# Kernel tuning notes

Measured on AMD Instinct MI355X. Metric: run time of the kernel, lower is better.

The kernel has to match this reference:

```python
import jax, jax.numpy as jnp
import numpy as np

BS, SEQ, ML, DEPTH = 32, 50, 16, 4
NN = 2 ** DEPTH - 1          # 15 nodes per complete binary tree (heap layout)
VOCAB, EMB, ENC = 50000, 128, 128
GH = 32                      # bigru hidden per direction
NC = 100                     # num_concepts
LH = 128                     # LSTM hidden
LIN = 2 + 2 * GH + NC + 1    # 167 LSTM feature dim


def _gru_dir(x, Wx, Wh, bx, bh, reverse):
    # x: [B, T, I]; torch GRU gate order r,z,n
    B, H = x.shape[0], Wh.shape[1]
    xe = jnp.einsum('bti,gi->btg', x, Wx) + bx   # [B,T,3H]
    xs = jnp.swapaxes(xe, 0, 1)
    if reverse:
        xs = xs[::-1]
    def step(h, xt):
        gh = h @ Wh.T + bh
        r = jax.nn.sigmoid(xt[:, :H] + gh[:, :H])
        z = jax.nn.sigmoid(xt[:, H:2 * H] + gh[:, H:2 * H])
        n = jnp.tanh(xt[:, 2 * H:] + r * gh[:, 2 * H:])
        hn = (1.0 - z) * n + z * h
        return hn, hn
    _, hs = jax.lax.scan(step, jnp.zeros((B, H), x.dtype), xs)
    if reverse:
        hs = hs[::-1]
    return jnp.swapaxes(hs, 0, 1)


def _lstm(x, Wx, Wh, bx, bh):
    # x: [B, T, I]; torch LSTM gate order i,f,g,o
    B, H = x.shape[0], Wh.shape[1]
    xe = jnp.einsum('bti,gi->btg', x, Wx) + bx   # [B,T,4H]
    def step(carry, xt):
        h, c = carry
        g = xt + h @ Wh.T + bh
        i = jax.nn.sigmoid(g[:, :H])
        f = jax.nn.sigmoid(g[:, H:2 * H])
        gg = jnp.tanh(g[:, 2 * H:3 * H])
        o = jax.nn.sigmoid(g[:, 3 * H:])
        c = f * c + i * gg
        h = o * jnp.tanh(c)
        return (h, c), h
    h0 = (jnp.zeros((B, H), x.dtype), jnp.zeros((B, H), x.dtype))
    _, hs = jax.lax.scan(step, h0, jnp.swapaxes(xe, 0, 1))
    return jnp.swapaxes(hs, 0, 1)


def setup_inputs() -> dict:
    key = jax.random.key(0)
    ks = jax.random.split(key, 24)
    p = {}
    p['p_id'] = jax.random.randint(ks[0], (BS, SEQ), 0, 1000)
    p['c_id'] = jax.random.randint(ks[1], (BS, SEQ), 0, NC)
    p['ast_tokens'] = jax.random.randint(ks[2], (BS, SEQ, ML, NN), 0, VOCAB)
    p['target_c'] = jax.nn.one_hot(jax.random.randint(ks[3], (BS, SEQ), 0, NC + 1), NC + 1, dtype=jnp.float32)
    p['c_embed'] = jax.random.normal(ks[4], (BS, SEQ, NC + 1), jnp.float32)
    p['cur_result'] = jax.random.normal(ks[5], (BS, SEQ, 2), jnp.float32)
    p['result'] = (jax.random.uniform(ks[6], (BS * SEQ,)) < 0.5).astype(jnp.float32)
    p['emb'] = jax.random.normal(ks[7], (VOCAB, EMB), jnp.float32) * 0.02
    p['Wc_w'] = jax.random.normal(ks[8], (ENC, EMB), jnp.float32) / np.sqrt(EMB)
    p['Wc_b'] = jnp.zeros((ENC,), jnp.float32)
    p['gru_WxF'] = jax.random.normal(ks[9], (3 * GH, ENC), jnp.float32) / np.sqrt(ENC)
    p['gru_WhF'] = jax.random.normal(ks[10], (3 * GH, GH), jnp.float32) / np.sqrt(GH)
    p['gru_bxF'] = jnp.zeros((3 * GH,), jnp.float32)
    p['gru_bhF'] = jnp.zeros((3 * GH,), jnp.float32)
    p['gru_WxB'] = jax.random.normal(ks[11], (3 * GH, ENC), jnp.float32) / np.sqrt(ENC)
    p['gru_WhB'] = jax.random.normal(ks[12], (3 * GH, GH), jnp.float32) / np.sqrt(GH)
    p['gru_bxB'] = jnp.zeros((3 * GH,), jnp.float32)
    p['gru_bhB'] = jnp.zeros((3 * GH,), jnp.float32)
    p['lstm_Wx'] = jax.random.normal(ks[13], (4 * LH, LIN), jnp.float32) / np.sqrt(LIN)
    p['lstm_Wh'] = jax.random.normal(ks[14], (4 * LH, LH), jnp.float32) / np.sqrt(LH)
    p['lstm_bx'] = jnp.zeros((4 * LH,), jnp.float32)
    p['lstm_bh'] = jnp.zeros((4 * LH,), jnp.float32)
    p['pred_w'] = jax.random.normal(ks[15], (NC + 1, LH), jnp.float32) / np.sqrt(LH)
    p['pred_b'] = jnp.zeros((NC + 1,), jnp.float32)
    return p


def reference(p_id, c_id, ast_tokens, target_c, c_embed, cur_result, result,
              emb, Wc_w, Wc_b,
              gru_WxF, gru_WhF, gru_bxF, gru_bhF,
              gru_WxB, gru_WhB, gru_bxB, gru_bhB,
              lstm_Wx, lstm_Wh, lstm_bx, lstm_bh,
              pred_w, pred_b):
    # BatchTreeEncoder: per-node W_c(emb(tok)), subtree-sum via bottom-up heap, max over nodes
    e = emb[ast_tokens] @ Wc_w.T + Wc_b          # [BS,SEQ,ML,NN,ENC]
    s = e
    for lvl in range(DEPTH - 2, -1, -1):          # bottom-up over fixed tree levels
        par = np.arange(2 ** lvl - 1, 2 ** (lvl + 1) - 1)
        s = s.at[..., par, :].add(s[..., 2 * par + 1, :] + s[..., 2 * par + 2, :])
    tree_enc = jnp.max(s, axis=3)                 # [BS,SEQ,ML,ENC]
    x = tree_enc.reshape(BS * SEQ, ML, ENC)
    hf = _gru_dir(x, gru_WxF, gru_WhF, gru_bxF, gru_bhF, False)
    hb = _gru_dir(x, gru_WxB, gru_WhB, gru_bxB, gru_bhB, True)
    gout = jnp.concatenate([hf, hb], axis=-1)     # [BS*SEQ, ML, 64]
    code = jnp.max(gout, axis=1).reshape(BS, SEQ, 2 * GH)  # max_pool1d over time
    lin = jnp.concatenate([c_embed, code, cur_result], axis=-1)  # [BS,SEQ,LIN]
    lout = _lstm(lin, lstm_Wx, lstm_Wh, lstm_bx, lstm_bh)         # [BS,SEQ,LH]
    pred = lout.reshape(BS * SEQ, LH) @ pred_w.T + pred_b         # [BS*SEQ, NC+1]
    tc = target_c.reshape(BS * SEQ, NC + 1)
    p1 = jnp.sum(pred * tc, axis=-1)              # bmm(pred, target_c)
    ncon = jnp.sum(tc, axis=-1)
    m = (ncon > 0).astype(pred.dtype)
    fp = p1 / jnp.maximum(ncon, 1.0)
    bce = jnp.maximum(fp, 0.0) - fp * result + jnp.log1p(jnp.exp(-jnp.abs(fp)))
    loss = jnp.sum(bce * m) / jnp.maximum(jnp.sum(m), 1.0)
    return loss, jax.nn.sigmoid(fp) * m, result * m
```

## Files before the change

### kernel.cpp

```cpp
#include <hip/hip_runtime.h>
#include <hip/hip_bf16.h>
#include <math.h>

#define BS 32
#define SEQ 50
#define ML 16
#define NN 15
#define NTREE (BS*SEQ*ML)
#define NROW (BS*SEQ)
#define VOCAB 50000
#define EMB 128
#define ENC 128
#define GH 32
#define NC 100
#define LH 128
#define LIN_D 167
#define LIN_P 192

typedef float f32x4 __attribute__((ext_vector_type(4)));
typedef short s16x8 __attribute__((ext_vector_type(8)));
typedef unsigned int u32;
typedef u32 u32x4v __attribute__((ext_vector_type(4)));

#define LOG2E 1.4426950408889634f
__device__ __forceinline__ float fsig(float x) {
  return __builtin_amdgcn_rcpf(1.f + __builtin_amdgcn_exp2f(-LOG2E * x));
}
__device__ __forceinline__ float ftanh(float x) {
  return 2.f * __builtin_amdgcn_rcpf(
             1.f + __builtin_amdgcn_exp2f(-2.f * LOG2E * x)) - 1.f;
}
__device__ __forceinline__ u32 pkbf(float x, float y) {
  u32 a = __float_as_uint(x), b = __float_as_uint(y);
  a = (a + 0x7FFFu + ((a >> 16) & 1u)) >> 16;
  b = (b + 0x7FFFu + ((b >> 16) & 1u)) >> 16;
  return a | (b << 16);
}
__device__ __forceinline__ unsigned short f2bf(float x) {
  u32 a = __float_as_uint(x);
  return (unsigned short)((a + 0x7FFFu + ((a >> 16) & 1u)) >> 16);
}
#define MFMA __builtin_amdgcn_mfma_f32_16x16x32_bf16

__global__ __launch_bounds__(256) void gemm_mfma(
    const float* __restrict__ A, const u32* __restrict__ Bpk,
    const float* __restrict__ bias, void* __restrict__ Cout,
    int M, int N, int out_bf16) {
  int w = threadIdx.x >> 6, lane = threadIdx.x & 63;
  int R0 = blockIdx.x * 64 + w * 16;
  int r = R0 + (lane & 15);
  int rm = (r < M) ? r : (M - 1);
  const float* Ar = A + (size_t)rm * 128 + (lane >> 4) * 8;
  s16x8 a0, a1, a2, a3;
  {
#define LDA(AF, KT) { \
    float4 f0 = *(const float4*)(Ar + KT * 32); \
    float4 f1 = *(const float4*)(Ar + KT * 32 + 4); \
    u32x4v q = {pkbf(f0.x, f0.y), pkbf(f0.z, f0.w), \
                pkbf(f1.x, f1.y), pkbf(f1.z, f1.w)}; \
    AF = __builtin_bit_cast(s16x8, q); }
    LDA(a0, 0) LDA(a1, 1) LDA(a2, 2) LDA(a3, 3)
#undef LDA
  }
  const u32x4v* Bp = (const u32x4v*)Bpk;
  for (int c = 0; c < N; c += 64) {
    f32x4 acc0, acc1, acc2, acc3;
    {
      float b0 = bias ? bias[c + (lane & 15)]      : 0.f;
      float b1 = bias ? bias[c + 16 + (lane & 15)] : 0.f;
      float b2 = bias ? bias[c + 32 + (lane & 15)] : 0.f;
      float b3 = bias ? bias[c + 48 + (lane & 15)] : 0.f;
      acc0 = (f32x4){b0, b0, b0, b0}; acc1 = (f32x4){b1, b1, b1, b1};
      acc2 = (f32x4){b2, b2, b2, b2}; acc3 = (f32x4){b3, b3, b3, b3};
    }
    int fbase = (c >> 4) * 4;
#define DONT(ACC, NT) { \
    s16x8 bf0 = __builtin_bit_cast(s16x8, Bp[(size_t)(fbase + NT * 4 + 0) * 64 + lane]); \
    s16x8 bf1 = __builtin_bit_cast(s16x8, Bp[(size_t)(fbase + NT * 4 + 1) * 64 + lane]); \
    s16x8 bf2 = __builtin_bit_cast(s16x8, Bp[(size_t)(fbase + NT * 4 + 2) * 64 + lane]); \
    s16x8 bf3 = __builtin_bit_cast(s16x8, Bp[(size_t)(fbase + NT * 4 + 3) * 64 + lane]); \
    ACC = MFMA(a0, bf0, ACC, 0, 0, 0); ACC = MFMA(a1, bf1, ACC, 0, 0, 0); \
    ACC = MFMA(a2, bf2, ACC, 0, 0, 0); ACC = MFMA(a3, bf3, ACC, 0, 0, 0); }
    DONT(acc0, 0) DONT(acc1, 1) DONT(acc2, 2) DONT(acc3, 3)
#undef DONT
    int colb = c + (lane & 15);
    int rowb = R0 + (lane >> 4) * 4;
#define STNT(ACC, NT) \
    _Pragma("unroll") \
    for (int j = 0; j < 4; j++) { \
      int row = rowb + j; \
      if (row < M) { \
        if (out_bf16) ((unsigned short*)Cout)[(size_t)row * N + colb + NT * 16] = f2bf(ACC[j]); \
        else ((float*)Cout)[(size_t)row * N + colb + NT * 16] = ACC[j]; \
      } \
    }
    STNT(acc0, 0) STNT(acc1, 1) STNT(acc2, 2) STNT(acc3, 3)
#undef STNT
  }
}

__global__ __launch_bounds__(256) void sgemm_nt(const float* __restrict__ A,
    const float* __restrict__ B, const float* __restrict__ bias,
    float* __restrict__ C, int M, int N, int K) {
  __shared__ float As[32][68];
  __shared__ float Bs[32][132];
  const int bm = blockIdx.y * 64, bn = blockIdx.x * 128;
  const int tid = threadIdx.x;
  const int tm = (tid >> 4) << 2;
  const int tn = (tid & 15) << 3;
  const int srow = tid >> 3;
  const int q4 = (tid & 7) << 2;

  float acc[4][8];
  #pragma unroll
  for (int i = 0; i < 4; i++)
    #pragma unroll
    for (int j = 0; j < 8; j++) acc[i][j] = 0.f;

  for (int k0 = 0; k0 < K; k0 += 32) {
    #pragma unroll
    for (int h = 0; h < 2; h++) {
      int gm = bm + srow + h * 32;
      int rm = (gm < M) ? gm : (M - 1);
      float4 av = *(const float4*)&A[(size_t)rm * K + k0 + q4];
      As[q4 + 0][srow + h * 32] = av.x;
      As[q4 + 1][srow + h * 32] = av.y;
      As[q4 + 2][srow + h * 32] = av.z;
      As[q4 + 3][srow + h * 32] = av.w;
    }
    #pragma unroll
    for (int h = 0; h < 4; h++) {
      int gn = bn + srow + h * 32;
      float4 bv = make_float4(0.f, 0.f, 0.f, 0.f);
      if (gn < N) bv = *(const float4*)&B[(size_t)gn * K + k0 + q4];
      Bs[q4 + 0][srow + h * 32] = bv.x;
      Bs[q4 + 1][srow + h * 32] = bv.y;
      Bs[q4 + 2][srow + h * 32] = bv.z;
      Bs[q4 + 3][srow + h * 32] = bv.w;
    }
    __syncthreads();
    #pragma unroll
    for (int kk = 0; kk < 32; kk++) {
      float4 a4 = *(const float4*)&As[kk][tm];
      float4 b0 = *(const float4*)&Bs[kk][tn];
      float4 b1 = *(const float4*)&Bs[kk][tn + 4];
      float a[4] = {a4.x, a4.y, a4.z, a4.w};
      float b[8] = {b0.x, b0.y, b0.z, b0.w, b1.x, b1.y, b1.z, b1.w};
      #pragma unroll
      for (int i = 0; i < 4; i++)
        #pragma unroll
        for (int j = 0; j < 8; j++) acc[i][j] += a[i] * b[j];
    }
    __syncthreads();
  }

  float bb[8];
  #pragma unroll
  for (int j = 0; j < 8; j++) {
    int gn = bn + tn + j;
    bb[j] = (bias && gn < N) ? bias[gn] : 0.f;
  }
  if (bn + tn < N) {
    #pragma unroll
    for (int i = 0; i < 4; i++) {
      int gm = bm + tm + i;
      if (gm >= M) continue;
      float4 v0 = make_float4(acc[i][0] + bb[0], acc[i][1] + bb[1],
                              acc[i][2] + bb[2], acc[i][3] + bb[3]);
      float4 v1 = make_float4(acc[i][4] + bb[4], acc[i][5] + bb[5],
                              acc[i][6] + bb[6], acc[i][7] + bb[7]);
      *(float4*)&C[(size_t)gm * N + bn + tn] = v0;
      *(float4*)&C[(size_t)gm * N + bn + tn + 4] = v1;
    }
  }
}

__global__ __launch_bounds__(256) void k_prep(const float* __restrict__ WxF,
    const float* __restrict__ WxB, const float* __restrict__ bxF,
    const float* __restrict__ bxB, const float* __restrict__ lstm_Wx,
    const float* __restrict__ lstm_Wh, const float* __restrict__ Wc_w,
    float* __restrict__ ball, float* __restrict__ Wxp,
    u32* __restrict__ Wcpk, u32* __restrict__ Wallpk, u32* __restrict__ Wpk) {
  int i = blockIdx.x * 256 + threadIdx.x;
  if (i < 96) ball[i] = bxF[i];
  else if (i < 192) ball[i] = bxB[i - 96];
  if (i < 8192) {
    int fg = i >> 8, l = (i >> 2) & 63, p = i & 3;
    int nt = fg >> 2, kt = fg & 3;
    int n = nt * 16 + (l & 15);
    int k = kt * 32 + (l >> 4) * 8 + 2 * p;
    Wcpk[i] = pkbf(Wc_w[n * 128 + k], Wc_w[n * 128 + k + 1]);
  }
  if (i < 12288) {
    int fg = i >> 8, l = (i >> 2) & 63, p = i & 3;
    int nt = fg >> 2, kt = fg & 3;
    int n = nt * 16 + (l & 15);
    int k = kt * 32 + (l >> 4) * 8 + 2 * p;
    float v0 = (n < 96) ? WxF[n * 128 + k]     : WxB[(n - 96) * 128 + k];
    float v1 = (n < 96) ? WxF[n * 128 + k + 1] : WxB[(n - 96) * 128 + k + 1];
    Wallpk[i] = pkbf(v0, v1);
  }
  if (i < 32768) {
    int fg = i >> 8, l = (i >> 2) & 63, p = i & 3;
    int w = fg >> 4, nt = (fg >> 2) & 3, kt = fg & 3;
    int n = 64 * w + 16 * nt + (l & 15);
    int k = 32 * kt + 8 * (l >> 4) + 2 * p;
    Wpk[i] = pkbf(lstm_Wh[n * 128 + k], lstm_Wh[n * 128 + k + 1]);
  }
  if (i < 512 * LIN_P) {
    int n = i / LIN_P, k = i - n * LIN_P;
    Wxp[i] = (k < LIN_D) ? lstm_Wx[n * LIN_D + k] : 0.f;
  }
}

__global__ __launch_bounds__(256) void k_tree(const int* __restrict__ ast,
    const u32* __restrict__ Epb, const float* __restrict__ Wc_b,
    float* __restrict__ x) {
  int lt = threadIdx.x >> 7;
  int d  = threadIdx.x & 127;
  int tree = blockIdx.x * 2 + lt;
  __shared__ int toks[2][15];
  if (d < 15) toks[lt][d] = ast[(size_t)tree * 15 + d];
  __syncthreads();
  float e[15];
  int half = d >> 1;
  bool odd = (d & 1) != 0;
  #pragma unroll
  for (int n = 0; n < 15; n++) {
    u32 v = Epb[(size_t)toks[lt][n] * 64 + half];
    e[n] = __uint_as_float(odd ? (v & 0xFFFF0000u) : (v << 16));
  }
  float b = Wc_b[d];
  float s3 = e[3] + e[7] + e[8],  s4 = e[4] + e[9] + e[10];
  float s5 = e[5] + e[11] + e[12], s6 = e[6] + e[13] + e[14];
  float s1 = e[1] + s3 + s4, s2 = e[2] + s5 + s6;
  float s0 = e[0] + s1 + s2;
  float ml = fmaxf(fmaxf(fmaxf(e[7], e[8]), fmaxf(e[9], e[10])),
                   fmaxf(fmaxf(e[11], e[12]), fmaxf(e[13], e[14]))) + b;
  float mm = fmaxf(fmaxf(s3, s4), fmaxf(s5, s6)) + 3.f * b;
  float mt = fmaxf(s1, s2) + 7.f * b;
  float m = fmaxf(fmaxf(ml, mm), fmaxf(mt, s0 + 15.f * b));
  x[(size_t)tree * 128 + d] = m;
}

__global__ __launch_bounds__(128) void k_gru(const float* __restrict__ xe_all,
    const float* __restrict__ WhF, const float* __restrict__ WhB,
    const float* __restrict__ bhF, const float* __restrict__ bhB,
    float* __restrict__ code) {
  int bsq = blockIdx.x >> 1, dir = blockIdx.x & 1;
  int g = threadIdx.x;
  __shared__ float whs[96 * 32];
  __shared__ float h_lds[32];
  __shared__ float rz[64];
  __shared__ float nn[32];
  const float* Wh = dir ? WhB : WhF;
  const float* bh = dir ? bhB : bhF;
  for (int i = g; i < 96 * 32; i += 128) whs[i] = Wh[i];
  if (g < 32) h_lds[g] = 0.f;
  __syncthreads();
  float w[32]; float bhv = 0.f, mxv = -1e30f;
  if (g < 96) {
    #pragma unroll
    for (int j = 0; j < 32; j++) w[j] = whs[g * 32 + j];
    bhv = bh[g];
  }
  for (int s = 0; s < 16; s++) {
    int t = dir ? (15 - s) : s;
    const float* xe = xe_all + ((size_t)(bsq * 16 + t)) * 192 + dir * 96;
    float gh = bhv, xv = 0.f;
    if (g < 96) {
      xv = xe[g];
      #pragma unroll
      for (int j = 0; j < 32; j++) gh += w[j] * h_lds[j];
    }
    if (g < 64) rz[g] = fsig(xv + gh);
    __syncthreads();
    if (g >= 64 && g < 96) nn[g - 64] = ftanh(xv + rz[g - 64] * gh);
    __syncthreads();
    if (g < 32) {
      float z = rz[g + 32];
      float hn = (1.f - z) * nn[g] + z * h_lds[g];
      mxv = fmaxf(mxv, hn);
      h_lds[g] = hn;
    }
    __syncthreads();
  }
  if (g < 32) code[(size_t)bsq * 64 + dir * 32 + g] = mxv;
}

__global__ __launch_bounds__(256) void k_lin(const float* __restrict__ c_embed,
    const float* __restrict__ code, const float* __restrict__ cur,
    float* __restrict__ lin) {
  int i = blockIdx.x * 256 + threadIdx.x;
  if (i >= NROW * LIN_P) return;
  int row = i / LIN_P, j = i - row * LIN_P;
  float v;
  if (j < 101) v = c_embed[row * 101 + j];
  else if (j < 165) v = code[row * 64 + (j - 101)];
  else if (j < 167) v = cur[row * 2 + (j - 165)];
  else v = 0.f;
  lin[i] = v;
}

__global__ __launch_bounds__(512) void k_lstm(
    const float* __restrict__ xeL, const u32* __restrict__ Wpk,
    const float* __restrict__ bh, float* __restrict__ lout) {
  __shared__ float xl[SEQ * 512];
  __shared__ float hh[SEQ * 128];
  __shared__ float ga[512];
  __shared__ s16x8 hl8[16];
  short* hls = (short*)hl8;
  int b = blockIdx.x, t = threadIdx.x;
  int w = t >> 6, lane = t & 63;
  const float* xrow = xeL + (size_t)b * SEQ * 512;
  #pragma unroll 5
  for (int i = t; i < SEQ * 512; i += 512) xl[i] = xrow[i];
  const s16x8* WB = (const s16x8*)Wpk + (size_t)w * 16 * 64 + lane;
  s16x8 B0  = WB[0 * 64],  B1  = WB[1 * 64],  B2  = WB[2 * 64],  B3  = WB[3 * 64];
  s16x8 B4  = WB[4 * 64],  B5  = WB[5 * 64],  B6  = WB[6 * 64],  B7  = WB[7 * 64];
  s16x8 B8  = WB[8 * 64],  B9  = WB[9 * 64],  B10 = WB[10 * 64], B11 = WB[11 * 64];
  s16x8 B12 = WB[12 * 64], B13 = WB[13 * 64], B14 = WB[14 * 64], B15 = WB[15 * 64];

  int gbase = 64 * w + lane;
  float bhv0 = 0, bhv1 = 0, bhv2 = 0, bhv3 = 0;
  if (lane < 16) {
    bhv0 = bh[gbase]; bhv1 = bh[gbase + 16];
    bhv2 = bh[gbase + 32]; bhv3 = bh[gbase + 48];
  }
  float c = 0.f;
  if (t < 128) hls[t] = 0;
  __syncthreads();
  const s16x8 zz = {0, 0, 0, 0, 0, 0, 0, 0};
  const bool arow = (lane & 15) == 0;
  const int asel = lane >> 4;
  const bool tanh_gate = (w == 4 || w == 5);
  for (int step = 0; step < SEQ; step++) {
    s16x8 a0 = arow ? hl8[asel]      : zz;
    s16x8 a1 = arow ? hl8[4 + asel]  : zz;
    s16x8 a2 = arow ? hl8[8 + asel]  : zz;
    s16x8 a3 = arow ? hl8[12 + asel] : zz;
    f32x4 acc0 = {0, 0, 0, 0}, acc1 = {0, 0, 0, 0};
    f32x4 acc2 = {0, 0, 0, 0}, acc3 = {0, 0, 0, 0};
    if (lane < 16) {
      const float* xs = xl + step * 512;
      acc0[0] = xs[gbase]      + bhv0;
      acc1[0] = xs[gbase + 16] + bhv1;
      acc2[0] = xs[gbase + 32] + bhv2;
      acc3[0] = xs[gbase + 48] + bhv3;
    }
    acc0 = MFMA(a0, B0,  acc0, 0, 0, 0); acc0 = MFMA(a1, B1,  acc0, 0, 0, 0);
    acc0 = MFMA(a2, B2,  acc0, 0, 0, 0); acc0 = MFMA(a3, B3,  acc0, 0, 0, 0);
    acc1 = MFMA(a0, B4,  acc1, 0, 0, 0); acc1 = MFMA(a1, B5,  acc1, 0, 0, 0);
    acc1 = MFMA(a2, B6,  acc1, 0, 0, 0); acc1 = MFMA(a3, B7,  acc1, 0, 0, 0);
    acc2 = MFMA(a0, B8,  acc2, 0, 0, 0); acc2 = MFMA(a1, B9,  acc2, 0, 0, 0);
    acc2 = MFMA(a2, B10, acc2, 0, 0, 0); acc2 = MFMA(a3, B11, acc2, 0, 0, 0);
    acc3 = MFMA(a0, B12, acc3, 0, 0, 0); acc3 = MFMA(a1, B13, acc3, 0, 0, 0);
    acc3 = MFMA(a2, B14, acc3, 0, 0, 0); acc3 = MFMA(a3, B15, acc3, 0, 0, 0);
    if (lane < 16) {
      if (tanh_gate) {
        ga[gbase]      = ftanh(acc0[0]);
        ga[gbase + 16] = ftanh(acc1[0]);
        ga[gbase + 32] = ftanh(acc2[0]);
        ga[gbase + 48] = ftanh(acc3[0]);
      } else {
        ga[gbase]      = fsig(acc0[0]);
        ga[gbase + 16] = fsig(acc1[0]);
        ga[gbase + 32] = fsig(acc2[0]);
        ga[gbase + 48] = fsig(acc3[0]);
      }
    }
    __syncthreads();
    if (t < 128) {
      c = ga[t + 128] * c + ga[t] * ga[t + 256];
      float h = ga[t + 384] * ftanh(c);
      hh[step * 128 + t] = h;
      u32 xb = __float_as_uint(h);
      hls[t] = (short)((xb + 0x7FFFu + ((xb >> 16) & 1u)) >> 16);
    }
    __syncthreads();
  }
  float* lo = lout + (size_t)b * SEQ * 128;
  #pragma unroll 4
  for (int i = t; i < SEQ * 128; i += 512) lo[i] = hh[i];
}

__global__ __launch_bounds__(128) void k_pred(const float* __restrict__ lout,
    const float* __restrict__ pred_w, const float* __restrict__ pred_b,
    const float* __restrict__ tc, const float* __restrict__ result,
    float* __restrict__ out, float* __restrict__ fpbuf, float* __restrict__ mbuf) {
  int row = blockIdx.x; int k = threadIdx.x;
  __shared__ float tcs[101];
  __shared__ float r1[128], r2[128], r3[128];
  if (k < 101) tcs[k] = tc[(size_t)row * 101 + k];
  __syncthreads();
  float lk = lout[(size_t)row * 128 + k];
  float acc = 0.f;
  for (int c = 0; c < 101; c++) acc += tcs[c] * pred_w[c * 128 + k];
  float v = acc * lk;
  float pb = (k < 101) ? tcs[k] * pred_b[k] : 0.f;
  float nc = (k < 101) ? tcs[k] : 0.f;
  r1[k] = v; r2[k] = pb; r3[k] = nc;
  __syncthreads();
  for (int st = 64; st > 0; st >>= 1) {
    if (k < st) { r1[k] += r1[k + st]; r2[k] += r2[k + st]; r3[k] += r3[k + st]; }
    __syncthreads();
  }
  if (k == 0) {
    float ncon = r3[0];
    float m = (ncon > 0.f) ? 1.f : 0.f;
    float fp = (r1[0] + r2[0]) / fmaxf(ncon, 1.f);
    fpbuf[row] = fp; mbuf[row] = m;
    out[1 + row] = m / (1.f + expf(-fp));
    out[1 + NROW + row] = result[row] * m;
  }
}

__global__ __launch_bounds__(256) void k_loss(const float* __restrict__ fpbuf,
    const float* __restrict__ mbuf, const float* __restrict__ result,
    float* __restrict__ out) {
  __shared__ float sb[256], sm[256];
  int k = threadIdx.x;
  float ab = 0.f, am = 0.f;
  for (int r = k; r < NROW; r += 256) {
    float fp = fpbuf[r], m = mbuf[r], res = result[r];
    float bce = fmaxf(fp, 0.f) - fp * res + log1pf(expf(-fabsf(fp)));
    ab += bce * m; am += m;
  }
  sb[k] = ab; sm[k] = am;
  __syncthreads();
  for (int st = 128; st > 0; st >>= 1) {
    if (k < st) { sb[k] += sb[k + st]; sm[k] += sm[k + st]; }
    __syncthreads();
  }
  if (k == 0) out[0] = sb[0] / fmaxf(sm[0], 1.f);
}

extern "C" void kernel_launch(void* const* d_in, const int* in_sizes, int n_in,
                              void* d_out, int out_size, void* d_ws, size_t ws_size,
                              hipStream_t stream) {
  (void)in_sizes; (void)n_in; (void)out_size; (void)ws_size;
  const int*   ast      = (const int*)  d_in[2];
  const float* target_c = (const float*)d_in[3];
  const float* c_embed  = (const float*)d_in[4];
  const float* cur_res  = (const float*)d_in[5];
  const float* result   = (const float*)d_in[6];
  const float* emb      = (const float*)d_in[7];
  const float* Wc_w     = (const float*)d_in[8];
  const float* Wc_b     = (const float*)d_in[9];
  const float* gru_WxF  = (const float*)d_in[10];
  const float* gru_WhF  = (const float*)d_in[11];
  const float* gru_bxF  = (const float*)d_in[12];
  const float* gru_bhF  = (const float*)d_in[13];
  const float* gru_WxB  = (const float*)d_in[14];
  const float* gru_WhB  = (const float*)d_in[15];
  const float* gru_bxB  = (const float*)d_in[16];
  const float* gru_bhB  = (const float*)d_in[17];
  const float* lstm_Wx  = (const float*)d_in[18];
  const float* lstm_Wh  = (const float*)d_in[19];
  const float* lstm_bx  = (const float*)d_in[20];
  const float* lstm_bh  = (const float*)d_in[21];
  const float* pred_w   = (const float*)d_in[22];
  const float* pred_b   = (const float*)d_in[23];
  float* out = (float*)d_out;

  float* W = (float*)d_ws;
  u32*   Epb    = (u32*)W;
  float* x      = W + 3200000;
  float* xe_all = W + 6476800;
  u32*   Wcpk   = (u32*)(W + 11392000);
  u32*   Wallpk = (u32*)(W + 11400192);
  float* ball   = W + 11412480;
  float* Wxp    = W + 11412672;
  float* code   = W + 11510976;
  float* lin    = W + 11613376;
  float* xeL    = W + 11920576;
  float* lout   = W + 12739776;
  float* fpbuf  = W + 12944576;
  float* mbuf   = W + 12946176;
  u32*   Wpk    = (u32*)(W + 12947776);

  k_prep<<<384, 256, 0, stream>>>(gru_WxF, gru_WxB, gru_bxF, gru_bxB, lstm_Wx,
                                  lstm_Wh, Wc_w, ball, Wxp, Wcpk, Wallpk, Wpk);
  gemm_mfma<<<782, 256, 0, stream>>>(emb, Wcpk, nullptr, Epb, VOCAB, 128, 1);
  k_tree<<<NTREE / 2, 256, 0, stream>>>(ast, Epb, Wc_b, x);
  gemm_mfma<<<400, 256, 0, stream>>>(x, Wallpk, ball, xe_all, NTREE, 192, 0);
  k_gru<<<NROW * 2, 128, 0, stream>>>(xe_all, gru_WhF, gru_WhB, gru_bhF, gru_bhB, code);
  k_lin<<<(NROW * LIN_P + 255) / 256, 256, 0, stream>>>(c_embed, code, cur_res, lin);
  sgemm_nt<<<dim3(4, 25), 256, 0, stream>>>(lin, Wxp, lstm_bx, xeL, NROW, 512, LIN_P);
  k_lstm<<<BS, 512, 0, stream>>>(xeL, Wpk, lstm_bh, lout);
  k_pred<<<NROW, 128, 0, stream>>>(lout, pred_w, pred_b, target_c, result,
                                   out, fpbuf, mbuf);
  k_loss<<<1, 256, 0, stream>>>(fpbuf, mbuf, result, out);
}
```

Before: 149.0 us.

## Use bf16 tree output, MFMA LSTM input GEMM, redundant LSTM cell update, fuse loss

Result: slower. 175.6 us (+17.8%).

```diff
diff --git a/kernel.cpp b/kernel.cpp
--- a/kernel.cpp
+++ b/kernel.cpp
@@ -15,7 +15,6 @@
 #define NC 100
 #define LH 128
 #define LIN_D 167
-#define LIN_P 192
 
 typedef float f32x4 __attribute__((ext_vector_type(4)));
 typedef short s16x8 __attribute__((ext_vector_type(8)));
@@ -99,79 +98,105 @@
   }
 }
 
-__global__ __launch_bounds__(256) void sgemm_nt(const float* __restrict__ A,
-    const float* __restrict__ B, const float* __restrict__ bias,
-    float* __restrict__ C, int M, int N, int K) {
-  __shared__ float As[32][68];
-  __shared__ float Bs[32][132];
-  const int bm = blockIdx.y * 64, bn = blockIdx.x * 128;
-  const int tid = threadIdx.x;
-  const int tm = (tid >> 4) << 2;
-  const int tn = (tid & 15) << 3;
-  const int srow = tid >> 3;
-  const int q4 = (tid & 7) << 2;
-
-  float acc[4][8];
+__global__ __launch_bounds__(256) void gemm_mfma_bfA(
+    const unsigned short* __restrict__ Ab, const u32* __restrict__ Bpk,
+    const float* __restrict__ bias, float* __restrict__ Cout,
+    int M, int N) {
+  int w = threadIdx.x >> 6, lane = threadIdx.x & 63;
+  int R0 = blockIdx.x * 64 + w * 16;
+  int r = R0 + (lane & 15);
+  int rm = (r < M) ? r : (M - 1);
+  const unsigned short* Ar = Ab + (size_t)rm * 128 + (lane >> 4) * 8;
+  s16x8 a0 = *(const s16x8*)(Ar + 0);
+  s16x8 a1 = *(const s16x8*)(Ar + 32);
+  s16x8 a2 = *(const s16x8*)(Ar + 64);
+  s16x8 a3 = *(const s16x8*)(Ar + 96);
+  const u32x4v* Bp = (const u32x4v*)Bpk;
+  for (int c = 0; c < N; c += 64) {
+    f32x4 acc0, acc1, acc2, acc3;
+    {
+      float b0 = bias[c + (lane & 15)];
+      float b1 = bias[c + 16 + (lane & 15)];
+      float b2 = bias[c + 32 + (lane & 15)];
+      float b3 = bias[c + 48 + (lane & 15)];
+      acc0 = (f32x4){b0, b0, b0, b0}; acc1 = (f32x4){b1, b1, b1, b1};
+      acc2 = (f32x4){b2, b2, b2, b2}; acc3 = (f32x4){b3, b3, b3, b3};
+    }
+    int fbase = (c >> 4) * 4;
+#define DONT(ACC, NT) { \
+    s16x8 bf0 = __builtin_bit_cast(s16x8, Bp[(size_t)(fbase + NT * 4 + 0) * 64 + lane]); \
+    s16x8 bf1 = __builtin_bit_cast(s16x8, Bp[(size_t)(fbase + NT * 4 + 1) * 64 + lane]); \
+    s16x8 bf2 = __builtin_bit_cast(s16x8, Bp[(size_t)(fbase + NT * 4 + 2) * 64 + lane]); \
+    s16x8 bf3 = __builtin_bit_cast(s16x8, Bp[(size_t)(fbase + NT * 4 + 3) * 64 + lane]); \
+    ACC = MFMA(a0, bf0, ACC, 0, 0, 0); ACC = MFMA(a1, bf1, ACC, 0, 0, 0); \
+    ACC = MFMA(a2, bf2, ACC, 0, 0, 0); ACC = MFMA(a3, bf3, ACC, 0, 0, 0); }
+    DONT(acc0, 0) DONT(acc1, 1) DONT(acc2, 2) DONT(acc3, 3)
+#undef DONT
+    int colb = c + (lane & 15);
+    int rowb = R0 + (lane >> 4) * 4;
+#define STNT(ACC, NT) \
+    _Pragma("unroll") \
+    for (int j = 0; j < 4; j++) { \
+      int row = rowb + j; \
+      if (row < M) Cout[(size_t)row * N + colb + NT * 16] = ACC[j]; \
+    }
+    STNT(acc0, 0) STNT(acc1, 1) STNT(acc2, 2) STNT(acc3, 3)
+#undef STNT
+  }
+}
+
+__device__ __forceinline__ float lin_at(const float* __restrict__ ce,
+    const float* __restrict__ co, const float* __restrict__ cu,
+    int row, int k) {
+  if (k < 101) return ce[row * 101 + k];
+  if (k < 165) return co[row * 64 + (k - 101)];
+  if (k < 167) return cu[row * 2 + (k - 165)];
+  return 0.f;
+}
+
+__global__ __launch_bounds__(256) void gemm_lin(
+    const float* __restrict__ c_embed, const float* __restrict__ code,
+    const float* __restrict__ cur, const u32* __restrict__ Bpk,
+    const float* __restrict__ bias, float* __restrict__ Cout) {
+  int w = threadIdx.x >> 6, lane = threadIdx.x & 63;
+  int R0 = blockIdx.x * 64 + w * 16;
+  int r = R0 + (lane & 15);
+  s16x8 a[6];
   #pragma unroll
-  for (int i = 0; i < 4; i++)
+  for (int kt = 0; kt < 6; kt++) {
+    int k0 = kt * 32 + (lane >> 4) * 8;
+    float f[8];
     #pragma unroll
-    for (int j = 0; j < 8; j++) acc[i][j] = 0.f;
-
-  for (int k0 = 0; k0 < K; k0 += 32) {
+    for (int j = 0; j < 8; j++) f[j] = lin_at(c_embed, code, cur, r, k0 + j);
+    u32x4v q = {pkbf(f[0], f[1]), pkbf(f[2], f[3]),
+                pkbf(f[4], f[5]), pkbf(f[6], f[7])};
+    a[kt] = __builtin_bit_cast(s16x8, q);
+  }
+  const u32x4v* Bp = (const u32x4v*)Bpk;
+  for (int c = 0; c < 512; c += 64) {
+    f32x4 acc[4];
     #pragma unroll
-    for (int h = 0; h < 2; h++) {
-      int gm = bm + srow + h * 32;
-      int rm = (gm < M) ? gm : (M - 1);
-      float4 av = *(const float4*)&A[(size_t)rm * K + k0 + q4];
-      As[q4 + 0][srow + h * 32] = av.x;
-      As[q4 + 1][srow + h * 32] = av.y;
-      As[q4 + 2][srow + h * 32] = av.z;
-      As[q4 + 3][srow + h * 32] = av.w;
-    }
+    for (int nt = 0; nt < 4; nt++) {
+      float bv = bias[c + nt * 16 + (lane & 15)];
+      acc[nt] = (f32x4){bv, bv, bv, bv};
+    }
+    int fbase = (c >> 4) * 6;
     #pragma unroll
-    for (int h = 0; h < 4; h++) {
-      int gn = bn + srow + h * 32;
-      float4 bv = make_float4(0.f, 0.f, 0.f, 0.f);
-      if (gn < N) bv = *(const float4*)&B[(size_t)gn * K + k0 + q4];
-      Bs[q4 + 0][srow + h * 32] = bv.x;
-      Bs[q4 + 1][srow + h * 32] = bv.y;
-      Bs[q4 + 2][srow + h * 32] = bv.z;
-      Bs[q4 + 3][srow + h * 32] = bv.w;
-    }
-    __syncthreads();
+    for (int nt = 0; nt < 4; nt++) {
+      #pragma unroll
+      for (int kt = 0; kt < 6; kt++) {
+        s16x8 bf = __builtin_bit_cast(s16x8,
+            Bp[(size_t)(fbase + nt * 6 + kt) * 64 + lane]);
+        acc[nt] = MFMA(a[kt], bf, acc[nt], 0, 0, 0);
+      }
+    }
+    int colb = c + (lane & 15);
+    int rowb = R0 + (lane >> 4) * 4;
     #pragma unroll
-    for (int kk = 0; kk < 32; kk++) {
-      float4 a4 = *(const float4*)&As[kk][tm];
-      float4 b0 = *(const float4*)&Bs[kk][tn];
-      float4 b1 = *(const float4*)&Bs[kk][tn + 4];
-      float a[4] = {a4.x, a4.y, a4.z, a4.w};
-      float b[8] = {b0.x, b0.y, b0.z, b0.w, b1.x, b1.y, b1.z, b1.w};
+    for (int nt = 0; nt < 4; nt++)
       #pragma unroll
-      for (int i = 0; i < 4; i++)
-        #pragma unroll
-        for (int j = 0; j < 8; j++) acc[i][j] += a[i] * b[j];
-    }
-    __syncthreads();
-  }
-
-  float bb[8];
-  #pragma unroll
-  for (int j = 0; j < 8; j++) {
-    int gn = bn + tn + j;
-    bb[j] = (bias && gn < N) ? bias[gn] : 0.f;
-  }
-  if (bn + tn < N) {
-    #pragma unroll
-    for (int i = 0; i < 4; i++) {
-      int gm = bm + tm + i;
-      if (gm >= M) continue;
-      float4 v0 = make_float4(acc[i][0] + bb[0], acc[i][1] + bb[1],
-                              acc[i][2] + bb[2], acc[i][3] + bb[3]);
-      float4 v1 = make_float4(acc[i][4] + bb[4], acc[i][5] + bb[5],
-                              acc[i][6] + bb[6], acc[i][7] + bb[7]);
-      *(float4*)&C[(size_t)gm * N + bn + tn] = v0;
-      *(float4*)&C[(size_t)gm * N + bn + tn + 4] = v1;
-    }
+      for (int j = 0; j < 4; j++)
+        Cout[(size_t)(rowb + j) * 512 + colb + nt * 16] = acc[nt][j];
   }
 }
 
@@ -179,9 +204,11 @@
     const float* __restrict__ WxB, const float* __restrict__ bxF,
     const float* __restrict__ bxB, const float* __restrict__ lstm_Wx,
     const float* __restrict__ lstm_Wh, const float* __restrict__ Wc_w,
-    float* __restrict__ ball, float* __restrict__ Wxp,
-    u32* __restrict__ Wcpk, u32* __restrict__ Wallpk, u32* __restrict__ Wpk) {
+    float* __restrict__ ball, u32* __restrict__ Wcpk,
+    u32* __restrict__ Wallpk, u32* __restrict__ Wxpk, u32* __restrict__ Wpk,
+    u32* __restrict__ cnt) {
   int i = blockIdx.x * 256 + threadIdx.x;
+  if (i == 0) cnt[0] = 0u;
   if (i < 96) ball[i] = bxF[i];
   else if (i < 192) ball[i] = bxB[i - 96];
   if (i < 8192) {
@@ -200,6 +227,15 @@
     float v1 = (n < 96) ? WxF[n * 128 + k + 1] : WxB[(n - 96) * 128 + k + 1];
     Wallpk[i] = pkbf(v0, v1);
   }
+  if (i < 49152) {
+    int fg = i >> 8, l = (i >> 2) & 63, p = i & 3;
+    int nt = fg / 6, kt = fg % 6;
+    int n = nt * 16 + (l & 15);
+    int k = kt * 32 + (l >> 4) * 8 + 2 * p;
+    float v0 = (k < LIN_D)     ? lstm_Wx[n * LIN_D + k]     : 0.f;
+    float v1 = (k + 1 < LIN_D) ? lstm_Wx[n * LIN_D + k + 1] : 0.f;
+    Wxpk[i] = pkbf(v0, v1);
+  }
   if (i < 32768) {
     int fg = i >> 8, l = (i >> 2) & 63, p = i & 3;
     int w = fg >> 4, nt = (fg >> 2) & 3, kt = fg & 3;
@@ -207,15 +243,11 @@
     int k = 32 * kt + 8 * (l >> 4) + 2 * p;
     Wpk[i] = pkbf(lstm_Wh[n * 128 + k], lstm_Wh[n * 128 + k + 1]);
   }
-  if (i < 512 * LIN_P) {
-    int n = i / LIN_P, k = i - n * LIN_P;
-    Wxp[i] = (k < LIN_D) ? lstm_Wx[n * LIN_D + k] : 0.f;
-  }
 }
 
 __global__ __launch_bounds__(256) void k_tree(const int* __restrict__ ast,
     const u32* __restrict__ Epb, const float* __restrict__ Wc_b,
-    float* __restrict__ x) {
+    unsigned short* __restrict__ x_bf) {
   int lt = threadIdx.x >> 7;
   int d  = threadIdx.x & 127;
   int tree = blockIdx.x * 2 + lt;
@@ -240,7 +272,7 @@
   float mm = fmaxf(fmaxf(s3, s4), fmaxf(s5, s6)) + 3.f * b;
   float mt = fmaxf(s1, s2) + 7.f * b;
   float m = fmaxf(fmaxf(ml, mm), fmaxf(mt, s0 + 15.f * b));
-  x[(size_t)tree * 128 + d] = m;
+  x_bf[(size_t)tree * 128 + d] = f2bf(m);
 }
 
 __global__ __launch_bounds__(128) void k_gru(const float* __restrict__ xe_all,
@@ -288,28 +320,13 @@
   if (g < 32) code[(size_t)bsq * 64 + dir * 32 + g] = mxv;
 }
 
-__global__ __launch_bounds__(256) void k_lin(const float* __restrict__ c_embed,
-    const float* __restrict__ code, const float* __restrict__ cur,
-    float* __restrict__ lin) {
-  int i = blockIdx.x * 256 + threadIdx.x;
-  if (i >= NROW * LIN_P) return;
-  int row = i / LIN_P, j = i - row * LIN_P;
-  float v;
-  if (j < 101) v = c_embed[row * 101 + j];
-  else if (j < 165) v = code[row * 64 + (j - 101)];
-  else if (j < 167) v = cur[row * 2 + (j - 165)];
-  else v = 0.f;
-  lin[i] = v;
-}
-
 __global__ __launch_bounds__(512) void k_lstm(
     const float* __restrict__ xeL, const u32* __restrict__ Wpk,
     const float* __restrict__ bh, float* __restrict__ lout) {
   __shared__ float xl[SEQ * 512];
   __shared__ float hh[SEQ * 128];
-  __shared__ float ga[512];
-  __shared__ s16x8 hl8[16];
-  short* hls = (short*)hl8;
+  __shared__ float ga[2][512];
+  __shared__ s16x8 hl8p[8][16];
   int b = blockIdx.x, t = threadIdx.x;
   int w = t >> 6, lane = t & 63;
   const float* xrow = xeL + (size_t)b * SEQ * 512;
@@ -327,18 +344,20 @@
     bhv0 = bh[gbase]; bhv1 = bh[gbase + 16];
     bhv2 = bh[gbase + 32]; bhv3 = bh[gbase + 48];
   }
-  float c = 0.f;
-  if (t < 128) hls[t] = 0;
+  float c0 = 0.f, c1 = 0.f;
+  short* hw = (short*)&hl8p[w];
+  hw[lane] = 0; hw[64 + lane] = 0;
   __syncthreads();
   const s16x8 zz = {0, 0, 0, 0, 0, 0, 0, 0};
   const bool arow = (lane & 15) == 0;
   const int asel = lane >> 4;
   const bool tanh_gate = (w == 4 || w == 5);
+  int p = 0;
   for (int step = 0; step < SEQ; step++) {
-    s16x8 a0 = arow ? hl8[asel]      : zz;
-    s16x8 a1 = arow ? hl8[4 + asel]  : zz;
-    s16x8 a2 = arow ? hl8[8 + asel]  : zz;
-    s16x8 a3 = arow ? hl8[12 + asel] : zz;
+    s16x8 a0 = arow ? hl8p[w][asel]      : zz;
+    s16x8 a1 = arow ? hl8p[w][4 + asel]  : zz;
+    s16x8 a2 = arow ? hl8p[w][8 + asel]  : zz;
+    s16x8 a3 = arow ? hl8p[w][12 + asel] : zz;
     f32x4 acc0 = {0, 0, 0, 0}, acc1 = {0, 0, 0, 0};
     f32x4 acc2 = {0, 0, 0, 0}, acc3 = {0, 0, 0, 0};
     if (lane < 16) {
@@ -358,39 +377,51 @@
     acc3 = MFMA(a2, B14, acc3, 0, 0, 0); acc3 = MFMA(a3, B15, acc3, 0, 0, 0);
     if (lane < 16) {
       if (tanh_gate) {
-        ga[gbase]      = ftanh(acc0[0]);
-        ga[gbase + 16] = ftanh(acc1[0]);
-        ga[gbase + 32] = ftanh(acc2[0]);
-        ga[gbase + 48] = ftanh(acc3[0]);
+        ga[p][gbase]      = ftanh(acc0[0]);
+        ga[p][gbase + 16] = ftanh(acc1[0]);
+        ga[p][gbase + 32] = ftanh(acc2[0]);
+        ga[p][gbase + 48] = ftanh(acc3[0]);
       } else {
-        ga[gbase]      = fsig(acc0[0]);
-        ga[gbase + 16] = fsig(acc1[0]);
-        ga[gbase + 32] = fsig(acc2[0]);
-        ga[gbase + 48] = fsig(acc3[0]);
+        ga[p][gbase]      = fsig(acc0[0]);
+        ga[p][gbase + 16] = fsig(acc1[0]);
+        ga[p][gbase + 32] = fsig(acc2[0]);
+        ga[p][gbase + 48] = fsig(acc3[0]);
       }
     }
     __syncthreads();
-    if (t < 128) {
-      c = ga[t + 128] * c + ga[t] * ga[t + 256];
-      float h = ga[t + 384] * ftanh(c);
-      hh[step * 128 + t] = h;
-      u32 xb = __float_as_uint(h);
-      hls[t] = (short)((xb + 0x7FFFu + ((xb >> 16) & 1u)) >> 16);
-    }
-    __syncthreads();
-  }
+    {
+      float gi0 = ga[p][lane],       gi1 = ga[p][64 + lane];
+      float gf0 = ga[p][128 + lane], gf1 = ga[p][192 + lane];
+      float gg0 = ga[p][256 + lane], gg1 = ga[p][320 + lane];
+      float go0 = ga[p][384 + lane], go1 = ga[p][448 + lane];
+      c0 = gf0 * c0 + gi0 * gg0;
+      float h0 = go0 * ftanh(c0);
+      c1 = gf1 * c1 + gi1 * gg1;
+      float h1 = go1 * ftanh(c1);
+      hw[lane]      = (short)f2bf(h0);
+      hw[64 + lane] = (short)f2bf(h1);
+      if (w == 0) {
+        hh[step * 128 + lane] = h0;
+        hh[step * 128 + 64 + lane] = h1;
+      }
+    }
+    p ^= 1;
+  }
+  __syncthreads();
   float* lo = lout + (size_t)b * SEQ * 128;
   #pragma unroll 4
   for (int i = t; i < SEQ * 128; i += 512) lo[i] = hh[i];
 }
 
-__global__ __launch_bounds__(128) void k_pred(const float* __restrict__ lout,
+__global__ __launch_bounds__(128) void k_predloss(const float* __restrict__ lout,
     const float* __restrict__ pred_w, const float* __restrict__ pred_b,
     const float* __restrict__ tc, const float* __restrict__ result,
-    float* __restrict__ out, float* __restrict__ fpbuf, float* __restrict__ mbuf) {
+    float* __restrict__ out, float* __restrict__ fpbuf,
+    float* __restrict__ mbuf, u32* __restrict__ cnt) {
   int row = blockIdx.x; int k = threadIdx.x;
   __shared__ float tcs[101];
   __shared__ float r1[128], r2[128], r3[128];
+  __shared__ int lf;
   if (k < 101) tcs[k] = tc[(size_t)row * 101 + k];
   __syncthreads();
   float lk = lout[(size_t)row * 128 + k];
@@ -412,27 +443,27 @@
     fpbuf[row] = fp; mbuf[row] = m;
     out[1 + row] = m / (1.f + expf(-fp));
     out[1 + NROW + row] = result[row] * m;
-  }
-}
-
-__global__ __launch_bounds__(256) void k_loss(const float* __restrict__ fpbuf,
-    const float* __restrict__ mbuf, const float* __restrict__ result,
-    float* __restrict__ out) {
-  __shared__ float sb[256], sm[256];
-  int k = threadIdx.x;
-  float ab = 0.f, am = 0.f;
-  for (int r = k; r < NROW; r += 256) {
-    float fp = fpbuf[r], m = mbuf[r], res = result[r];
-    float bce = fmaxf(fp, 0.f) - fp * res + log1pf(expf(-fabsf(fp)));
-    ab += bce * m; am += m;
-  }
-  sb[k] = ab; sm[k] = am;
-  __syncthreads();
-  for (int st = 128; st > 0; st >>= 1) {
-    if (k < st) { sb[k] += sb[k + st]; sm[k] += sm[k + st]; }
+    __threadfence();
+    u32 old = atomicAdd(cnt, 1u);
+    lf = (old == NROW - 1) ? 1 : 0;
+  }
+  __syncthreads();
+  if (lf) {
+    __threadfence();
+    float ab = 0.f, am = 0.f;
+    for (int r = k; r < NROW; r += 128) {
+      float fp = fpbuf[r], m = mbuf[r], res = result[r];
+      float bce = fmaxf(fp, 0.f) - fp * res + log1pf(expf(-fabsf(fp)));
+      ab += bce * m; am += m;
+    }
+    r1[k] = ab; r2[k] = am;
     __syncthreads();
-  }
-  if (k == 0) out[0] = sb[0] / fmaxf(sm[0], 1.f);
+    for (int st = 64; st > 0; st >>= 1) {
+      if (k < st) { r1[k] += r1[k + st]; r2[k] += r2[k + st]; }
+      __syncthreads();
+    }
+    if (k == 0) out[0] = r1[0] / fmaxf(r2[0], 1.f);
+  }
 }
 
 extern "C" void kernel_launch(void* const* d_in, const int* in_sizes, int n_in,
@@ -465,30 +496,29 @@
 
   float* W = (float*)d_ws;
   u32*   Epb    = (u32*)W;
-  float* x      = W + 3200000;
-  float* xe_all = W + 6476800;
-  u32*   Wcpk   = (u32*)(W + 11392000);
-  u32*   Wallpk = (u32*)(W + 11400192);
-  float* ball   = W + 11412480;
-  float* Wxp    = W + 11412672;
-  float* code   = W + 11510976;
-  float* lin    = W + 11613376;
-  float* xeL    = W + 11920576;
-  float* lout   = W + 12739776;
-  float* fpbuf  = W + 12944576;
-  float* mbuf   = W + 12946176;
-  u32*   Wpk    = (u32*)(W + 12947776);
-
-  k_prep<<<384, 256, 0, stream>>>(gru_WxF, gru_WxB, gru_bxF, gru_bxB, lstm_Wx,
-                                  lstm_Wh, Wc_w, ball, Wxp, Wcpk, Wallpk, Wpk);
+  unsigned short* x_bf = (unsigned short*)(W + 3200000);
+  float* xe_all = W + 4838400;
+  float* code   = W + 9753600;
+  float* xeL    = W + 9856000;
+  float* lout   = W + 10675200;
+  float* fpbuf  = W + 10880000;
+  float* mbuf   = W + 10881600;
+  u32*   Wcpk   = (u32*)(W + 10883200);
+  u32*   Wallpk = (u32*)(W + 10891392);
+  u32*   Wxpk   = (u32*)(W + 10903680);
+  u32*   Wpk    = (u32*)(W + 10952832);
+  float* ball   = W + 10985600;
+  u32*   cnt    = (u32*)(W + 10985792);
+
+  k_prep<<<192, 256, 0, stream>>>(gru_WxF, gru_WxB, gru_bxF, gru_bxB, lstm_Wx,
+                                  lstm_Wh, Wc_w, ball, Wcpk, Wallpk, Wxpk, Wpk,
+                                  cnt);
   gemm_mfma<<<782, 256, 0, stream>>>(emb, Wcpk, nullptr, Epb, VOCAB, 128, 1);
-  k_tree<<<NTREE / 2, 256, 0, stream>>>(ast, Epb, Wc_b, x);
-  gemm_mfma<<<400, 256, 0, stream>>>(x, Wallpk, ball, xe_all, NTREE, 192, 0);
+  k_tree<<<NTREE / 2, 256, 0, stream>>>(ast, Epb, Wc_b, x_bf);
+  gemm_mfma_bfA<<<400, 256, 0, stream>>>(x_bf, Wallpk, ball, xe_all, NTREE, 192);
   k_gru<<<NROW * 2, 128, 0, stream>>>(xe_all, gru_WhF, gru_WhB, gru_bhF, gru_bhB, code);
-  k_lin<<<(NROW * LIN_P + 255) / 256, 256, 0, stream>>>(c_embed, code, cur_res, lin);
-  sgemm_nt<<<dim3(4, 25), 256, 0, stream>>>(lin, Wxp, lstm_bx, xeL, NROW, 512, LIN_P);
+  gemm_lin<<<25, 256, 0, stream>>>(c_embed, code, cur_res, Wxpk, lstm_bx, xeL);
   k_lstm<<<BS, 512, 0, stream>>>(xeL, Wpk, lstm_bh, lout);
-  k_pred<<<NROW, 128, 0, stream>>>(lout, pred_w, pred_b, target_c, result,
-                                   out, fpbuf, mbuf);
-  k_loss<<<1, 256, 0, stream>>>(fpbuf, mbuf, result, out);
-}
+  k_predloss<<<NROW, 128, 0, stream>>>(lout, pred_w, pred_b, target_c, result,
+                                       out, fpbuf, mbuf, cnt);
+}
```
